# Optimization experiments

Measured on AMD Instinct MI355X. Metric: run time of the kernel, lower is better.

## Reference

```python
import jax, jax.numpy as jnp
import numpy as np

N = 10000      # nodes
E = 160000     # directed edges (self loops added inside reference)
IN = 512       # input_len
HID = 256      # hidden per-head dim (hard-coded in module)
OUT = 128      # dim
H = 4          # heads
NEG_SLOPE = 0.2


def setup_inputs() -> dict:
    key = jax.random.key(0)
    ks = jax.random.split(key, 10)
    s = 0.05
    return {
        "x": jax.random.normal(ks[0], (N, IN), dtype=jnp.float32),
        "edge_index": jax.random.randint(ks[1], (2, E), 0, N, dtype=jnp.int64),
        # layer 1 params: GATv2Conv(IN, HID, heads=H, concat=False)
        "Wl1": jax.random.normal(ks[2], (IN, H * HID), dtype=jnp.float32) * s,
        "Wr1": jax.random.normal(ks[3], (IN, H * HID), dtype=jnp.float32) * s,
        "att1": jax.random.normal(ks[4], (H, HID), dtype=jnp.float32) * s,
        "b1": jnp.zeros((HID,), dtype=jnp.float32),
        # layer 2 params: GATv2Conv(HID, OUT, heads=H, concat=False)
        "Wl2": jax.random.normal(ks[5], (HID, H * OUT), dtype=jnp.float32) * s,
        "Wr2": jax.random.normal(ks[6], (HID, H * OUT), dtype=jnp.float32) * s,
        "att2": jax.random.normal(ks[7], (H, OUT), dtype=jnp.float32) * s,
        "b2": jnp.zeros((OUT,), dtype=jnp.float32),
    }


def gatv2_layer(x, src, dst, Wl, Wr, att, bias, num_nodes):
    """PyG GATv2Conv with concat=False (mean over heads), negative_slope=0.2."""
    heads, c = att.shape
    xl = (x @ Wl).reshape(num_nodes, heads, c)   # source transform
    xr = (x @ Wr).reshape(num_nodes, heads, c)   # target transform
    # per-edge attention logits: a^T LeakyReLU(xl[src] + xr[dst])  -> [E, H]
    e = jax.nn.leaky_relu(xl[src] + xr[dst], negative_slope=NEG_SLOPE)
    logits = jnp.einsum('ehc,hc->eh', e, att)
    # segment softmax over incoming edges of each destination node
    m = jax.ops.segment_max(logits, dst, num_segments=num_nodes)   # [N, H]
    ea = jnp.exp(logits - m[dst])
    denom = jax.ops.segment_sum(ea, dst, num_segments=num_nodes)   # [N, H]
    alpha = ea / denom[dst]                                        # [E, H]
    # scatter-aggregate messages
    out = jax.ops.segment_sum(alpha[:, :, None] * xl[src], dst, num_segments=num_nodes)
    return out.mean(axis=1) + bias                                 # [N, C]


def reference(x, edge_index, Wl1, Wr1, att1, b1, Wl2, Wr2, att2, b2):
    num_nodes = x.shape[0]
    loop = jnp.arange(num_nodes, dtype=edge_index.dtype)
    src = jnp.concatenate([edge_index[0], loop])
    dst = jnp.concatenate([edge_index[1], loop])
    h1 = jax.nn.leaky_relu(gatv2_layer(x, src, dst, Wl1, Wr1, att1, b1, num_nodes),
                           negative_slope=NEG_SLOPE)
    h2 = jnp.tanh(gatv2_layer(h1, src, dst, Wl2, Wr2, att2, b2, num_nodes))
    return h2
```

## Files before the change

### kernel.cpp

```cpp
#include <hip/hip_runtime.h>
#include <hip/hip_bf16.h>
#include <math.h>

#define DEVINL __device__ __forceinline__

typedef __attribute__((ext_vector_type(8))) short bf16x8;
typedef __attribute__((ext_vector_type(8))) unsigned short u16x8;
typedef __attribute__((ext_vector_type(4))) float f32x4;

DEVINL float lrelu(float x) { return x > 0.f ? x : 0.2f * x; }

DEVINL unsigned short f2bf_rne(float f) {
    unsigned u = __float_as_uint(f);
    unsigned r = u + 0x7fff + ((u >> 16) & 1);
    return (unsigned short)(r >> 16);
}
DEVINL float bf2f(unsigned short h) { return __uint_as_float(((unsigned)h) << 16); }

DEVINL void gload_lds16(const void* g, void* l) {
    __builtin_amdgcn_global_load_lds(
        (const __attribute__((address_space(1))) void*)g,
        (__attribute__((address_space(3))) void*)l, 16, 0, 0);
}


__global__ void build_edges(const int* __restrict__ ei, int E, int N,
                            int* __restrict__ src, int* __restrict__ dst,
                            int* __restrict__ counts) {
    int e = blockIdx.x * 256 + threadIdx.x;
    int ET = E + N;
    if (e >= ET) return;
    int s, d;
    if (e < E) { s = ei[e]; d = ei[E + e]; }
    else       { s = d = e - E; }
    s = min(max(s, 0), N - 1);
    d = min(max(d, 0), N - 1);
    src[e] = s;
    dst[e] = d;
    atomicAdd(&counts[d], 1);
}

__global__ void scan_offsets(const int* __restrict__ counts, int* __restrict__ offsets, int N) {
    const int T = 1024;
    __shared__ int sums[T];
    int t = threadIdx.x;
    int chunk = (N + T - 1) / T;
    int base = t * chunk;
    int local[16];
    int s = 0;
    for (int i = 0; i < chunk; ++i) {
        int v = (base + i < N) ? counts[base + i] : 0;
        local[i] = s;
        s += v;
    }
    sums[t] = s;
    __syncthreads();
    for (int d = 1; d < T; d <<= 1) {
        int v = (t >= d) ? sums[t - d] : 0;
        __syncthreads();
        sums[t] += v;
        __syncthreads();
    }
    int excl = (t == 0) ? 0 : sums[t - 1];
    for (int i = 0; i < chunk; ++i)
        if (base + i < N) offsets[base + i] = excl + local[i];
    if (t == T - 1) offsets[N] = excl + s;
}

__global__ void fill_eids(const int* __restrict__ src, const int* __restrict__ dst,
                          const int* __restrict__ offsets,
                          int* __restrict__ cursor, int* __restrict__ esrc, int ET) {
    int e = blockIdx.x * 256 + threadIdx.x;
    if (e >= ET) return;
    int d = dst[e];
    int pos = offsets[d] + atomicAdd(&cursor[d], 1);
    esrc[pos] = src[e];
}

__global__ void conv_hi(const float* __restrict__ x, unsigned short* __restrict__ hi,
                        int M, int log2K, int total4) {
    int i = blockIdx.x * 256 + threadIdx.x;
    if (i >= total4) return;
    int e = i * 4;
    int row = e >> log2K;
    ushort4 vh = make_ushort4(0, 0, 0, 0);
    if (row < M) {
        float4 v = *(const float4*)&x[e];
        vh = make_ushort4(f2bf_rne(v.x), f2bf_rne(v.y), f2bf_rne(v.z), f2bf_rne(v.w));
    }
    *(ushort4*)&hi[e] = vh;
}

__global__ void thi(const float* __restrict__ W, unsigned short* __restrict__ BTh,
                    int K, int Nout) {
    __shared__ float tile[32][33];
    int n0 = blockIdx.x * 32, k0 = blockIdx.y * 32;
    int tx = threadIdx.x, ty = threadIdx.y;
#pragma unroll
    for (int i = 0; i < 4; ++i)
        tile[ty + 8 * i][tx] = W[(size_t)(k0 + ty + 8 * i) * Nout + n0 + tx];
    __syncthreads();
#pragma unroll
    for (int i = 0; i < 4; ++i) {
        int r = ty + 8 * i;
        BTh[(size_t)(n0 + r) * K + k0 + tx] = f2bf_rne(tile[tx][r]);
    }
}

template <int TERMS, bool OUTBF16>
__global__ __launch_bounds__(256) void gemm_mfma(
    const unsigned short* __restrict__ Ah, const unsigned short* __restrict__ Al,
    const unsigned short* __restrict__ Bh,
    float* __restrict__ Cf, unsigned short* __restrict__ Cb,
    int M, int Nout, int K) {
    constexpr int BOFF = (TERMS == 2) ? 32768 : 16384;
    __shared__ __align__(16) char lds[BOFF + 16384];
    const int t = threadIdx.x;
    const int L = t & 63, w = t >> 6;
    const int wm = w & 1, wn = w >> 1;
    const int nwg = gridDim.x * gridDim.y;
    int orig = blockIdx.y * gridDim.x + blockIdx.x;
    int q = nwg >> 3, rr = nwg & 7;
    int xcd = orig & 7, pos = orig >> 3;
    int wg = (xcd < rr ? xcd * (q + 1) : rr * (q + 1) + (xcd - rr) * q) + pos;
    const int bm = (wg / gridDim.x) * 128, bn = (wg % gridDim.x) * 128;
    const size_t strideA = (size_t)K * 2;

    const f32x4 vzero = {0.f, 0.f, 0.f, 0.f};
    f32x4 acc[4][4];
#pragma unroll
    for (int i = 0; i < 4; ++i)
#pragma unroll
        for (int j = 0; j < 4; ++j) acc[i][j] = vzero;

    for (int k0 = 0; k0 < K; k0 += 64) {
#pragma unroll
        for (int i = 0; i < 4; ++i) {
            int slot = i * 256 + t;
            int offs = slot * 16;
            int r = offs >> 7;
            int cb = (offs & 127) ^ ((r & 7) << 4);
            size_t gofs = (size_t)r * strideA + (size_t)k0 * 2 + cb;
            gload_lds16((const char*)Ah + (size_t)bm * strideA + gofs, lds + offs);
            if constexpr (TERMS == 2)
                gload_lds16((const char*)Al + (size_t)bm * strideA + gofs, lds + 16384 + offs);
            gload_lds16((const char*)Bh + (size_t)bn * strideA + gofs, lds + BOFF + offs);
        }
        __syncthreads();
#pragma unroll
        for (int kf = 0; kf < 2; ++kf) {
            const int kb = kf * 64 + ((L >> 4) * 16);
            bf16x8 ah[4], al[4], bh[4];
#pragma unroll
            for (int mi = 0; mi < 4; ++mi) {
                int r = wm * 64 + mi * 16 + (L & 15);
                int off = r * 128 + (kb ^ ((r & 7) << 4));
                ah[mi] = *(const bf16x8*)(lds + off);
                if constexpr (TERMS == 2) al[mi] = *(const bf16x8*)(lds + 16384 + off);
            }
#pragma unroll
            for (int ni = 0; ni < 4; ++ni) {
                int r = wn * 64 + ni * 16 + (L & 15);
                int off = r * 128 + (kb ^ ((r & 7) << 4));
                bh[ni] = *(const bf16x8*)(lds + BOFF + off);
            }
#pragma unroll
            for (int mi = 0; mi < 4; ++mi)
#pragma unroll
                for (int ni = 0; ni < 4; ++ni) {
                    acc[mi][ni] = __builtin_amdgcn_mfma_f32_16x16x32_bf16(ah[mi], bh[ni], acc[mi][ni], 0, 0, 0);
                    if constexpr (TERMS == 2)
                        acc[mi][ni] = __builtin_amdgcn_mfma_f32_16x16x32_bf16(al[mi], bh[ni], acc[mi][ni], 0, 0, 0);
                }
        }
        __syncthreads();
    }
    const int colBase = bn + wn * 64 + (L & 15);
#pragma unroll
    for (int mi = 0; mi < 4; ++mi) {
        int row0 = bm + wm * 64 + mi * 16 + (L >> 4) * 4;
#pragma unroll
        for (int j = 0; j < 4; ++j) {
            int row = row0 + j;
            if (row < M) {
#pragma unroll
                for (int ni = 0; ni < 4; ++ni) {
                    if constexpr (OUTBF16)
                        Cb[(size_t)row * Nout + colBase + ni * 16] = f2bf_rne(acc[mi][ni][j]);
                    else
                        Cf[(size_t)row * Nout + colBase + ni * 16] = acc[mi][ni][j];
                }
            }
        }
    }
}

template <int C, int ACT, bool SPLIT, int RS>
__global__ __launch_bounds__(256) void fused_agg(const unsigned short* __restrict__ xl,
                                                 const unsigned short* __restrict__ xr,
                                                 const float* __restrict__ att,
                                                 const int* __restrict__ offsets,
                                                 const int* __restrict__ esrc,
                                                 const float* __restrict__ bias,
                                                 float* __restrict__ outF,
                                                 unsigned short* __restrict__ outH,
                                                 unsigned short* __restrict__ outL,
                                                 int N) {
    const int H = 4;
    constexpr int VEC = C / 16;
    __shared__ float accLds[H][C];
    int n = blockIdx.x;
    int t = threadIdx.x;
    if (SPLIT && n >= N) {
        if (t < C) {
            outH[(size_t)n * C + t] = 0;
            outL[(size_t)n * C + t] = 0;
        }
        return;
    }
    int h = t >> 6, lane = t & 63;
    int g = lane >> 4, gl = lane & 15;
    int o0 = offsets[n];
    int deg = offsets[n + 1] - o0;

    float a[VEC], r[VEC], acc[VEC];
    {
        const float* pa = att + h * C + gl * VEC;
#pragma unroll
        for (int v4 = 0; v4 < VEC / 4; ++v4) {
            float4 va = *(const float4*)(pa + v4 * 4);
            a[v4 * 4 + 0] = va.x; a[v4 * 4 + 1] = va.y;
            a[v4 * 4 + 2] = va.z; a[v4 * 4 + 3] = va.w;
        }
        const unsigned short* pr = xr + (size_t)n * RS + h * C + gl * VEC;
#pragma unroll
        for (int v8 = 0; v8 < VEC / 8; ++v8) {
            u16x8 u = *(const u16x8*)(pr + v8 * 8);
#pragma unroll
            for (int j = 0; j < 8; ++j) r[v8 * 8 + j] = bf2f(u[j]);
        }
    }
#pragma unroll
    for (int v = 0; v < VEC; ++v) acc[v] = 0.f;
    float s = 0.f;

    for (int j = g; j < deg; j += 4) {
        int sj = esrc[o0 + j];
        const unsigned short* px = xl + (size_t)sj * RS + h * C + gl * VEC;
        float xv[VEC];
#pragma unroll
        for (int v8 = 0; v8 < VEC / 8; ++v8) {
            u16x8 u = *(const u16x8*)(px + v8 * 8);
#pragma unroll
            for (int q = 0; q < 8; ++q) xv[v8 * 8 + q] = bf2f(u[q]);
        }
        float p = 0.f;
#pragma unroll
        for (int v = 0; v < VEC; ++v) p += a[v] * lrelu(xv[v] + r[v]);
        p += __shfl_xor(p, 1);
        p += __shfl_xor(p, 2);
        p += __shfl_xor(p, 4);
        p += __shfl_xor(p, 8);
        p = fminf(fmaxf(p, -60.f), 60.f);
        float wgt = __expf(p);
        s += wgt;
#pragma unroll
        for (int v = 0; v < VEC; ++v) acc[v] += wgt * xv[v];
    }
    s += __shfl_xor(s, 16);
    s += __shfl_xor(s, 32);
#pragma unroll
    for (int v = 0; v < VEC; ++v) {
        acc[v] += __shfl_xor(acc[v], 16);
        acc[v] += __shfl_xor(acc[v], 32);
    }

    if (g == 0) {
        float inv = 1.0f / s;
#pragma unroll
        for (int v = 0; v < VEC; ++v) accLds[h][gl * VEC + v] = acc[v] * inv;
    }
    __syncthreads();

    if (t < C) {
        float v = 0.f;
#pragma unroll
        for (int hh = 0; hh < H; ++hh) v += accLds[hh][t];
        v = v * 0.25f + bias[t];
        if (ACT == 0) v = lrelu(v);
        else          v = tanhf(v);
        if (SPLIT) {
            unsigned short hh16 = f2bf_rne(v);
            outH[(size_t)n * C + t] = hh16;
            outL[(size_t)n * C + t] = f2bf_rne(v - bf2f(hh16));
        } else {
            outF[(size_t)n * C + t] = v;
        }
    }
}


extern "C" void kernel_launch(void* const* d_in, const int* in_sizes, int n_in,
                              void* d_out, int out_size, void* d_ws, size_t ws_size,
                              hipStream_t stream) {
    const float* x    = (const float*)d_in[0];
    const int*   ei   = (const int*)d_in[1];
    const float* Wl1  = (const float*)d_in[2];
    const float* Wr1  = (const float*)d_in[3];
    const float* att1 = (const float*)d_in[4];
    const float* b1   = (const float*)d_in[5];
    const float* Wl2  = (const float*)d_in[6];
    const float* Wr2  = (const float*)d_in[7];
    const float* att2 = (const float*)d_in[8];
    const float* b2   = (const float*)d_in[9];
    float* out = (float*)d_out;

    const int IN = 512, HID = 256, OUT = 128, H = 4;
    int N  = in_sizes[0] / IN;
    int E  = in_sizes[1] / 2;
    int ET = E + N;
    int M2 = ((N + 127) / 128) * 128;

    char* w = (char*)d_ws;
    auto carve = [&](size_t bytes) {
        char* p = w;
        w += (bytes + 255) & ~(size_t)255;
        return (void*)p;
    };
    unsigned short* x_hi = (unsigned short*)carve((size_t)M2 * IN * 2);
    unsigned short* xlr1 = (unsigned short*)carve((size_t)N * 2 * H * HID * 2);
    unsigned short* BT1 = (unsigned short*)carve((size_t)(2 * H * HID) * IN * 2);
    int* src     = (int*)carve((size_t)ET * 4);
    int* dst     = (int*)carve((size_t)ET * 4);
    int* counts  = (int*)carve((size_t)N * 4);
    int* cursor  = (int*)carve((size_t)N * 4);
    int* offsets = (int*)carve((size_t)(N + 1) * 4);
    int* esrc    = (int*)carve((size_t)ET * 4);
    unsigned short* h1_h = x_hi;
    unsigned short* h1_l = x_hi + (size_t)M2 * HID;
    unsigned short* xlr2 = xlr1;
    unsigned short* BT2  = BT1;

    hipMemsetAsync(counts, 0, (size_t)((char*)offsets - (char*)counts), stream);
    build_edges<<<(ET + 255) / 256, 256, 0, stream>>>(ei, E, N, src, dst, counts);
    scan_offsets<<<1, 1024, 0, stream>>>(counts, offsets, N);
    fill_eids<<<(ET + 255) / 256, 256, 0, stream>>>(src, dst, offsets, cursor, esrc, ET);

    {
        int total4 = M2 * IN / 4;
        conv_hi<<<(total4 + 255) / 256, 256, 0, stream>>>(x, x_hi, N, 9, total4);
        thi<<<dim3((H * HID) / 32, IN / 32), dim3(32, 8), 0, stream>>>(Wl1, BT1, IN, H * HID);
        thi<<<dim3((H * HID) / 32, IN / 32), dim3(32, 8), 0, stream>>>(Wr1, BT1 + (size_t)(H * HID) * IN, IN, H * HID);
    }
    {
        dim3 g((2 * H * HID) / 128, M2 / 128);
        gemm_mfma<1, true><<<g, 256, 0, stream>>>(x_hi, nullptr, BT1, nullptr, xlr1, N, 2 * H * HID, IN);
    }
    fused_agg<256, 0, true, 2048><<<M2, 256, 0, stream>>>(xlr1, xlr1 + H * HID, att1, offsets, esrc, b1,
                                                          nullptr, h1_h, h1_l, N);
    thi<<<dim3((H * OUT) / 32, HID / 32), dim3(32, 8), 0, stream>>>(Wl2, BT2, HID, H * OUT);
    thi<<<dim3((H * OUT) / 32, HID / 32), dim3(32, 8), 0, stream>>>(Wr2, BT2 + (size_t)(H * OUT) * HID, HID, H * OUT);
    {
        dim3 g((2 * H * OUT) / 128, M2 / 128);
        gemm_mfma<2, true><<<g, 256, 0, stream>>>(h1_h, h1_l, BT2, nullptr, xlr2, N, 2 * H * OUT, HID);
    }
    fused_agg<128, 1, false, 1024><<<N, 256, 0, stream>>>(xlr2, xlr2 + H * OUT, att2, offsets, esrc, b2,
                                                          out, nullptr, nullptr, N);
}
```

Before: 208.4 us.

## Stage edge indices in LDS, process two edges per iteration, retune lane groups

The fused aggregation kernel now preloads up to 256 neighbor indices per node into shared memory. It then processes two edges per loop iteration so two independent row gathers are in flight at once. Layer 2 is switched to 8-lane groups instead of 16, so each group handles 16 channels and eight edges proceed in parallel per head. The goal is more memory-level parallelism for the latency-bound gathers, at the cost of more registers, an extra block barrier, and some wasted work on the padded second edge when the degree is odd.

```diff
diff --git a/kernel.cpp b/kernel.cpp
--- a/kernel.cpp
+++ b/kernel.cpp
@@ -195,7 +195,7 @@
     }
 }
 
-template <int C, int ACT, bool SPLIT, int RS>
+template <int C, int ACT, bool SPLIT, int RS, int LG2G>
 __global__ __launch_bounds__(256) void fused_agg(const unsigned short* __restrict__ xl,
                                                  const unsigned short* __restrict__ xr,
                                                  const float* __restrict__ att,
@@ -207,8 +207,12 @@
                                                  unsigned short* __restrict__ outL,
                                                  int N) {
     const int H = 4;
-    constexpr int VEC = C / 16;
+    constexpr int G   = 1 << LG2G;
+    constexpr int NG  = 64 >> LG2G;
+    constexpr int VEC = C / G;
+    constexpr int CAP = 256;
     __shared__ float accLds[H][C];
+    __shared__ int sEdge[CAP];
     int n = blockIdx.x;
     int t = threadIdx.x;
     if (SPLIT && n >= N) {
@@ -218,10 +222,15 @@
         }
         return;
     }
-    int h = t >> 6, lane = t & 63;
-    int g = lane >> 4, gl = lane & 15;
     int o0 = offsets[n];
     int deg = offsets[n + 1] - o0;
+
+    int dcap = min(deg, CAP);
+    for (int i = t; i < dcap; i += 256) sEdge[i] = esrc[o0 + i];
+    __syncthreads();
+
+    int h = t >> 6, lane = t & 63;
+    int g = lane >> LG2G, gl = lane & (G - 1);
 
     float a[VEC], r[VEC], acc[VEC];
     {
@@ -244,35 +253,49 @@
     for (int v = 0; v < VEC; ++v) acc[v] = 0.f;
     float s = 0.f;
 
-    for (int j = g; j < deg; j += 4) {
-        int sj = esrc[o0 + j];
-        const unsigned short* px = xl + (size_t)sj * RS + h * C + gl * VEC;
-        float xv[VEC];
+    for (int j = g; j < deg; j += 2 * NG) {
+        int j1 = j + NG;
+        bool has1 = j1 < deg;
+        int e0 = (j < CAP) ? sEdge[j] : esrc[o0 + j];
+        int jj = has1 ? j1 : j;
+        int e1 = (jj < CAP) ? sEdge[jj] : esrc[o0 + jj];
+        const unsigned short* p0 = xl + (size_t)e0 * RS + h * C + gl * VEC;
+        const unsigned short* p1 = xl + (size_t)e1 * RS + h * C + gl * VEC;
+        float x0[VEC], x1[VEC];
 #pragma unroll
         for (int v8 = 0; v8 < VEC / 8; ++v8) {
-            u16x8 u = *(const u16x8*)(px + v8 * 8);
-#pragma unroll
-            for (int q = 0; q < 8; ++q) xv[v8 * 8 + q] = bf2f(u[q]);
-        }
-        float p = 0.f;
-#pragma unroll
-        for (int v = 0; v < VEC; ++v) p += a[v] * lrelu(xv[v] + r[v]);
-        p += __shfl_xor(p, 1);
-        p += __shfl_xor(p, 2);
-        p += __shfl_xor(p, 4);
-        p += __shfl_xor(p, 8);
-        p = fminf(fmaxf(p, -60.f), 60.f);
-        float wgt = __expf(p);
-        s += wgt;
-#pragma unroll
-        for (int v = 0; v < VEC; ++v) acc[v] += wgt * xv[v];
-    }
-    s += __shfl_xor(s, 16);
-    s += __shfl_xor(s, 32);
-#pragma unroll
-    for (int v = 0; v < VEC; ++v) {
-        acc[v] += __shfl_xor(acc[v], 16);
-        acc[v] += __shfl_xor(acc[v], 32);
+            u16x8 u0 = *(const u16x8*)(p0 + v8 * 8);
+            u16x8 u1 = *(const u16x8*)(p1 + v8 * 8);
+#pragma unroll
+            for (int q = 0; q < 8; ++q) {
+                x0[v8 * 8 + q] = bf2f(u0[q]);
+                x1[v8 * 8 + q] = bf2f(u1[q]);
+            }
+        }
+        float q0 = 0.f, q1 = 0.f;
+#pragma unroll
+        for (int v = 0; v < VEC; ++v) {
+            q0 += a[v] * lrelu(x0[v] + r[v]);
+            q1 += a[v] * lrelu(x1[v] + r[v]);
+        }
+#pragma unroll
+        for (int m = 1; m < G; m <<= 1) {
+            q0 += __shfl_xor(q0, m);
+            q1 += __shfl_xor(q1, m);
+        }
+        q0 = fminf(fmaxf(q0, -60.f), 60.f);
+        q1 = fminf(fmaxf(q1, -60.f), 60.f);
+        float w0 = __expf(q0);
+        float w1 = has1 ? __expf(q1) : 0.f;
+        s += w0 + w1;
+#pragma unroll
+        for (int v = 0; v < VEC; ++v) acc[v] += w0 * x0[v] + w1 * x1[v];
+    }
+#pragma unroll
+    for (int m = G; m < 64; m <<= 1) {
+        s += __shfl_xor(s, m);
+#pragma unroll
+        for (int v = 0; v < VEC; ++v) acc[v] += __shfl_xor(acc[v], m);
     }
 
     if (g == 0) {
@@ -356,14 +379,14 @@
         dim3 g((2 * H * HID) / 128, M2 / 128);
         gemm_mfma<1, true><<<g, 256, 0, stream>>>(x_hi, nullptr, BT1, nullptr, xlr1, N, 2 * H * HID, IN);
     }
-    fused_agg<256, 0, true, 2048><<<M2, 256, 0, stream>>>(xlr1, xlr1 + H * HID, att1, offsets, esrc, b1,
-                                                          nullptr, h1_h, h1_l, N);
+    fused_agg<256, 0, true, 2048, 4><<<M2, 256, 0, stream>>>(xlr1, xlr1 + H * HID, att1, offsets, esrc, b1,
+                                                             nullptr, h1_h, h1_l, N);
     thi<<<dim3((H * OUT) / 32, HID / 32), dim3(32, 8), 0, stream>>>(Wl2, BT2, HID, H * OUT);
     thi<<<dim3((H * OUT) / 32, HID / 32), dim3(32, 8), 0, stream>>>(Wr2, BT2 + (size_t)(H * OUT) * HID, HID, H * OUT);
     {
         dim3 g((2 * H * OUT) / 128, M2 / 128);
         gemm_mfma<2, true><<<g, 256, 0, stream>>>(h1_h, h1_l, BT2, nullptr, xlr2, N, 2 * H * OUT, HID);
     }
-    fused_agg<128, 1, false, 1024><<<N, 256, 0, stream>>>(xlr2, xlr2 + H * OUT, att2, offsets, esrc, b2,
-                                                          out, nullptr, nullptr, N);
-}
+    fused_agg<128, 1, false, 1024, 3><<<N, 256, 0, stream>>>(xlr2, xlr2 + H * OUT, att2, offsets, esrc, b2,
+                                                             out, nullptr, nullptr, N);
+}
```

Result: slower. 219.2 us (+5.2%).
